# Kernel tuning notes

Hardware: AMD Instinct MI355X
Metric: run time of the kernel (lower is better)

The kernel has to match this reference:

```python
import jax, jax.numpy as jnp
import numpy as np

B, TK, NK, H, E, V = 128, 400, 50, 256, 256, 50000


def setup_inputs() -> dict:
    key = jax.random.key(0)
    ks = iter(jax.random.split(key, 48))
    def rn(shape, s=1.0):
        return jax.random.normal(next(ks), shape, jnp.float32) * s
    def ru(shape):
        return jax.random.uniform(next(ks), shape, jnp.float32)
    z = lambda shape: jnp.zeros(shape, jnp.float32)
    s = 0.05
    inp = {}
    inp['y_t_1'] = jax.random.randint(next(ks), (B,), 0, V)
    inp['h_prev'] = rn((B, H))
    inp['c_prev'] = rn((B, H))
    inp['encoder_outputs'] = rn((B, TK, H))
    inp['encoder_outputs_node'] = rn((B, NK, H))
    inp['enc_padding_mask'] = jnp.ones((B, TK), jnp.float32)
    inp['enc_padding_mask_node'] = jnp.ones((B, NK), jnp.float32)
    inp['c_t_d'] = rn((B, H))
    inp['c_t_g'] = rn((B, H))
    inp['c_t_g2'] = rn((B, H))
    inp['coverage'] = z((B, TK))
    inp['flow'] = ru((B, NK))
    inp['node_to_token'] = ru((B, NK, TK))
    inp['graph'] = ru((B, NK, NK))
    inp['voc_d'] = jax.random.randint(next(ks), (B, TK), 0, V)
    inp['step'] = 0
    # learned parameters
    inp['emb_table'] = rn((V, E), s)
    inp['Wx'] = rn((4 * H, E), s); inp['bx'] = z((E,))
    inp['Wi'] = rn((E, 4 * H), s); inp['Wh'] = rn((H, 4 * H), s)
    inp['bi'] = z((4 * H,)); inp['bh'] = z((4 * H,))
    inp['Whd'] = rn((H, H), s); inp['Wsd'] = rn((2 * H, H), s)
    inp['wcd'] = rn((H,), s); inp['vd'] = rn((H,), s); inp['bd'] = z((H,))
    inp['Wn'] = rn((H, H), s); inp['Wsf'] = rn((2 * H, H), s)
    inp['vf'] = rn((H,), s); inp['bf'] = z((H,))
    inp['Wpg'] = rn((5 * H + E, 1), s); inp['bpg'] = z((1,))
    inp['W1'] = rn((4 * H, H), s); inp['b1'] = z((H,))
    inp['W2'] = rn((H, V), s); inp['b2'] = z((V,))
    return inp


def _forward(y_t_1, h_prev, c_prev, enc, enc_n, mask_t, mask_n, c_t_d, c_t_g, c_t_g2,
             coverage, flow, n2t, graph, voc_d, emb_table, Wx, bx, Wi, Wh, bi, bh,
             Whd, Wsd, wcd, vd, bd, Wn, Wsf, vf, bf, Wpg, bpg, W1, b1, W2, b2):
    sig, tanh = jax.nn.sigmoid, jnp.tanh
    y_emb = emb_table[y_t_1]                                   # [B,E]
    x = jnp.concatenate([c_t_d, c_t_g, c_t_g2, y_emb], 1) @ Wx + bx
    # single-step LSTM (torch gate order i,f,g,o)
    gates = x @ Wi + h_prev @ Wh + bi + bh
    gi, gf, gg, go = jnp.split(gates, 4, axis=1)
    c_new = sig(gf) * c_prev + sig(gi) * tanh(gg)
    h_new = sig(go) * tanh(c_new)
    s_hat = jnp.concatenate([h_new, c_new], 1)                 # [B,2H]
    # doc attention with coverage (Bahdanau)
    e = tanh(enc @ Whd + (s_hat @ Wsd)[:, None, :] + coverage[:, :, None] * wcd + bd) @ vd
    a = jax.nn.softmax(e, axis=1) * mask_t
    a = a / a.sum(1, keepdims=True)                            # [B,TK]
    c_d = jnp.einsum('bt,bth->bh', a, enc)
    coverage_next = coverage + a
    # event-graph node attention (flow-weighted, one-hop propagation)
    en = tanh(enc_n @ Wn + (s_hat @ Wsf)[:, None, :] + bf) @ vf
    an = jax.nn.softmax(en, axis=1) * mask_n
    an = an / an.sum(1, keepdims=True)
    an = an * flow
    an = an / an.sum(1, keepdims=True)                         # [B,NK]
    c_g = jnp.einsum('bn,bnh->bh', an, enc_n)
    an2 = jnp.einsum('bn,bnm->bm', an, graph) * mask_n
    an2 = an2 / an2.sum(1, keepdims=True)
    c_g2 = jnp.einsum('bn,bnh->bh', an2, enc_n)
    a_n2t = jnp.einsum('bn,bnt->bt', an, n2t)
    a_n2t = a_n2t / a_n2t.sum(1, keepdims=True)
    # flow update: per-node max of token attention restricted to node tokens
    flow_ = jnp.max(a[:, None, :] * n2t, axis=2)               # [B,NK]
    flow_next = flow_ / flow_.sum(1, keepdims=True)
    # pointer-generator gate
    p_gen = sig(jnp.concatenate([c_d, c_g, c_g2, s_hat, x], 1) @ Wpg + bpg)  # [B,1]
    out = jnp.concatenate([h_new, c_d, c_g, c_g2], 1) @ W1 + b1
    vocab_dist = jax.nn.softmax(out @ W2 + b2, axis=1)         # [B,V]
    attn_all = a / a.sum(1, keepdims=True)
    attn_ = (1.0 - p_gen) * attn_all
    vocab_ = p_gen * vocab_dist
    rows = jnp.arange(vocab_.shape[0])[:, None]
    final_dist = vocab_.at[rows, voc_d].add(attn_)             # scatter_add over vocab
    return (final_dist, (h_new, c_new), c_d, c_g, c_g2, a, a_n2t, p_gen,
            coverage_next, flow_next)


def reference(y_t_1, h_prev, c_prev, encoder_outputs, encoder_outputs_node,
              enc_padding_mask, enc_padding_mask_node, c_t_d, c_t_g, c_t_g2,
              coverage, flow, node_to_token, graph, voc_d, step,
              emb_table, Wx, bx, Wi, Wh, bi, bh, Whd, Wsd, wcd, vd, bd,
              Wn, Wsf, vf, bf, Wpg, bpg, W1, b1, W2, b2):
    return _forward(y_t_1, h_prev, c_prev, encoder_outputs, encoder_outputs_node,
                    enc_padding_mask, enc_padding_mask_node, c_t_d, c_t_g, c_t_g2,
                    coverage, flow, node_to_token, graph, voc_d, emb_table, Wx, bx,
                    Wi, Wh, bi, bh, Whd, Wsd, wcd, vd, bd, Wn, Wsf, vf, bf,
                    Wpg, bpg, W1, b1, W2, b2)
```

## Files before the change

### kernel.cpp

```cpp
#include <hip/hip_runtime.h>
#include <stdint.h>


typedef unsigned short u16;
typedef unsigned int   u32;

#define Bv  128
#define TKv 400
#define NKv 50
#define Hv  256
#define Vv  50000
#define VPAD 50176
#define NSv 16
#define CHUNKv 3136

typedef __attribute__((ext_vector_type(8))) short bf16x8;
typedef __attribute__((ext_vector_type(4))) float f32x4;

__device__ float g_x[32768];
__device__ float g_xp[4 * 32768];
__device__ float g_gates[131072];
__device__ float g_h[32768];
__device__ float g_c[32768];
__device__ float g_sdp[2 * 32768];
__device__ float g_sfp[2 * 32768];
__device__ float g_e[51200];
__device__ float g_en[6400];
__device__ float g_a[51200];
__device__ float g_cd[32768];
__device__ float g_cdp[2 * 32768];
__device__ float g_cg[32768];
__device__ float g_cg2[32768];
__device__ float g_pg[128];
__device__ float g_o1[32768];
__device__ float g_vred[Bv * NSv * 2];
__device__ float g_logits[6400000];
__device__ u16   g_Wdt[256 * 256];
__device__ u16   g_Wnt[256 * 256];
__device__ u16   g_W2t[(size_t)VPAD * 256];

__device__ __forceinline__ float sigm(float x) { return 1.f / (1.f + expf(-x)); }

__device__ __forceinline__ u16 f2bf(float f) {
    u32 u = __float_as_uint(f);
    return (u16)((u + 0x7fffu + ((u >> 16) & 1u)) >> 16);
}

__device__ __forceinline__ bf16x8 cvt8(const float* __restrict__ p) {
    const float4 a = *(const float4*)p;
    const float4 b = *(const float4*)(p + 4);
    bf16x8 r;
    r[0] = (short)f2bf(a.x); r[1] = (short)f2bf(a.y);
    r[2] = (short)f2bf(a.z); r[3] = (short)f2bf(a.w);
    r[4] = (short)f2bf(b.x); r[5] = (short)f2bf(b.y);
    r[6] = (short)f2bf(b.z); r[7] = (short)f2bf(b.w);
    return r;
}

__device__ __forceinline__ float fast_tanh(float x) {
    x = fminf(fmaxf(x, -15.f), 15.f);
    float e = __expf(2.f * x);
    return (e - 1.f) / (e + 1.f);
}

__device__ __forceinline__ void ms_merge(float& m1, float& s1, float m2, float s2) {
    float M = fmaxf(m1, m2);
    s1 = s1 * expf(m1 - M) + s2 * expf(m2 - M);
    m1 = M;
}

__global__ __launch_bounds__(256) void k_tc(
    const float* __restrict__ src, u16* __restrict__ dst, int K, int N)
{
    __shared__ float tile[32][33];
    const int n0 = blockIdx.x * 32, k0 = blockIdx.y * 32;
    const int tx = threadIdx.x & 31, ty = threadIdx.x >> 5;
    #pragma unroll
    for (int i = 0; i < 32; i += 8) {
        int k = k0 + ty + i, n = n0 + tx;
        tile[ty + i][tx] = (n < N) ? src[(size_t)k * N + n] : 0.f;
    }
    __syncthreads();
    #pragma unroll
    for (int i = 0; i < 32; i += 8) {
        int n = n0 + ty + i, k = k0 + tx;
        dst[(size_t)n * K + k] = f2bf(tile[tx][ty + i]);
    }
}

__global__ __launch_bounds__(256) void k_x(
    const int* __restrict__ y,
    const float* __restrict__ ctd, const float* __restrict__ ctg,
    const float* __restrict__ ctg2, const float* __restrict__ emb,
    const float* __restrict__ Wx)
{
    const int b = blockIdx.x, ks = blockIdx.y, j = threadIdx.x;
    __shared__ float cs[256];
    float v;
    if      (ks == 0) v = ctd [b * 256 + j];
    else if (ks == 1) v = ctg [b * 256 + j];
    else if (ks == 2) v = ctg2[b * 256 + j];
    else              v = emb[(size_t)y[b] * 256 + j];
    cs[j] = v;
    __syncthreads();

    float acc = 0.f;
    const float* w = Wx + (size_t)(ks * 256) * 256 + j;
    #pragma unroll 8
    for (int k = 0; k < 256; k++) acc += cs[k] * w[(size_t)k * 256];
    g_xp[ks * 32768 + b * 256 + j] = acc;
}

__global__ __launch_bounds__(256) void k_gates(
    const float* __restrict__ h_prev,
    const float* __restrict__ Wi, const float* __restrict__ Wh,
    const float* __restrict__ bi, const float* __restrict__ bh,
    const float* __restrict__ bx)
{
    const int b = blockIdx.x, cc = blockIdx.y, j = threadIdx.x;
    __shared__ float xs[256], hs[256];

    float xv = bx[j] + g_xp[b * 256 + j] + g_xp[32768 + b * 256 + j]
             + g_xp[65536 + b * 256 + j] + g_xp[98304 + b * 256 + j];
    xs[j] = xv;
    if (cc == 0) g_x[b * 256 + j] = xv;
    hs[j] = h_prev[b * 256 + j];
    __syncthreads();

    const int col = cc * 256 + j;
    float acc = bi[col] + bh[col];
    const float* wi = Wi + col;
    const float* wh = Wh + col;
    #pragma unroll 8
    for (int k = 0; k < 256; k++)
        acc += xs[k] * wi[(size_t)k * 1024] + hs[k] * wh[(size_t)k * 1024];
    g_gates[b * 1024 + col] = acc;
}

__global__ __launch_bounds__(256) void k_cellsd(
    const float* __restrict__ c_prev,
    const float* __restrict__ Wsd, const float* __restrict__ Wsf,
    float* __restrict__ out_h, float* __restrict__ out_c)
{
    const int b = blockIdx.x, ks = blockIdx.y, j = threadIdx.x;
    __shared__ float sh[256];

    const float* gb = g_gates + b * 1024;
    float gi_ = gb[j], gf_ = gb[256 + j], gg_ = gb[512 + j], go_ = gb[768 + j];
    float cp = c_prev[b * 256 + j];
    float cn = sigm(gf_) * cp + sigm(gi_) * tanhf(gg_);
    float hn = sigm(go_) * tanhf(cn);
    if (ks == 0) {
        g_h[b * 256 + j] = hn;  g_c[b * 256 + j] = cn;
        out_h[b * 256 + j] = hn; out_c[b * 256 + j] = cn;
    }
    sh[j] = (ks == 0) ? hn : cn;
    __syncthreads();

    float asd = 0.f, asf = 0.f;
    const float* wd = Wsd + (size_t)(ks * 256) * 256 + j;
    const float* wf = Wsf + (size_t)(ks * 256) * 256 + j;
    #pragma unroll 8
    for (int k = 0; k < 256; k++) {
        float sv = sh[k];
        asd += sv * wd[(size_t)k * 256];
        asf += sv * wf[(size_t)k * 256];
    }
    g_sdp[ks * 32768 + b * 256 + j] = asd;
    g_sfp[ks * 32768 + b * 256 + j] = asf;
}

__global__ __launch_bounds__(256) void k_scores(
    const float* __restrict__ src, int R,
    const u16* __restrict__ Wt,
    const float* __restrict__ addv0,
    const float* __restrict__ addv1,
    const float* __restrict__ abias,
    const float* __restrict__ cov,
    const float* __restrict__ wcw,
    const float* __restrict__ vv,
    float* __restrict__ eout)
{
    const int b = blockIdx.y, t0 = blockIdx.x * 64;
    const int tid = threadIdx.x;
    const int lane = tid & 63, wave = tid >> 6;
    const int nlow = lane & 15, quad = lane >> 4;

    const u16* brow = Wt + (size_t)(wave * 64 + nlow) * 256 + quad * 8;

    bool tval[4]; const float* arow[4];
    #pragma unroll
    for (int mi = 0; mi < 4; mi++) {
        int trow = t0 + mi * 16 + nlow;
        tval[mi] = trow < R;
        arow[mi] = src + ((size_t)b * R + trow) * 256 + quad * 8;
    }

    const f32x4 zf = {0.f, 0.f, 0.f, 0.f};
    f32x4 acc[4][4];
    #pragma unroll
    for (int mi = 0; mi < 4; mi++)
        #pragma unroll
        for (int ni = 0; ni < 4; ni++) acc[mi][ni] = zf;

    for (int k0 = 0; k0 < 256; k0 += 32) {
        bf16x8 af[4], bf[4];
        #pragma unroll
        for (int mi = 0; mi < 4; mi++) {
            af[mi] = (bf16x8){0, 0, 0, 0, 0, 0, 0, 0};
            if (tval[mi]) af[mi] = cvt8(arow[mi] + k0);
        }
        #pragma unroll
        for (int ni = 0; ni < 4; ni++)
            bf[ni] = *(const bf16x8*)(brow + ni * 4096 + k0);
        #pragma unroll
        for (int mi = 0; mi < 4; mi++)
            #pragma unroll
            for (int ni = 0; ni < 4; ni++)
                acc[mi][ni] = __builtin_amdgcn_mfma_f32_16x16x32_bf16(
                    af[mi], bf[ni], acc[mi][ni], 0, 0, 0);
    }

    __shared__ float part[4][64];
    #pragma unroll
    for (int mi = 0; mi < 4; mi++) {
        float covt[4];
        #pragma unroll
        for (int r = 0; r < 4; r++) {
            int t = t0 + mi * 16 + quad * 4 + r;
            covt[r] = (cov && t < R) ? cov[b * R + t] : 0.f;
        }
        float s4[4] = {0.f, 0.f, 0.f, 0.f};
        #pragma unroll
        for (int ni = 0; ni < 4; ni++) {
            int col = wave * 64 + ni * 16 + nlow;
            float vvc = vv[col];
            float adc = addv0[b * 256 + col] + addv1[b * 256 + col] + abias[col];
            float wcc = wcw ? wcw[col] : 0.f;
            #pragma unroll
            for (int r = 0; r < 4; r++)
                s4[r] += vvc * fast_tanh(acc[mi][ni][r] + adc + covt[r] * wcc);
        }
        #pragma unroll
        for (int r = 0; r < 4; r++) {
            float s = s4[r];
            s += __shfl_xor(s, 1, 64);
            s += __shfl_xor(s, 2, 64);
            s += __shfl_xor(s, 4, 64);
            s += __shfl_xor(s, 8, 64);
            if (nlow == 0) part[wave][mi * 16 + quad * 4 + r] = s;
        }
    }
    __syncthreads();
    if (tid < 64) {
        int t = t0 + tid;
        if (t < R)
            eout[b * R + t] =
                part[0][tid] + part[1][tid] + part[2][tid] + part[3][tid];
    }
}

__global__ __launch_bounds__(256) void k_doc(
    const float* __restrict__ mask,
    const float* __restrict__ cov,
    float* __restrict__ out_a, float* __restrict__ out_cov)
{
    const int b = blockIdx.x, tid = threadIdx.x;
    __shared__ float red[256];

    float e0 = g_e[b * TKv + tid];
    float e1 = (tid + 256 < TKv) ? g_e[b * TKv + tid + 256] : -1e30f;

    float m = fmaxf(e0, e1);
    red[tid] = m; __syncthreads();
    for (int s = 128; s > 0; s >>= 1) { if (tid < s) red[tid] = fmaxf(red[tid], red[tid + s]); __syncthreads(); }
    m = red[0]; __syncthreads();

    float p0 = expf(e0 - m) * mask[b * TKv + tid];
    float p1 = (tid + 256 < TKv) ? expf(e1 - m) * mask[b * TKv + tid + 256] : 0.f;
    red[tid] = p0 + p1; __syncthreads();
    for (int s = 128; s > 0; s >>= 1) { if (tid < s) red[tid] += red[tid + s]; __syncthreads(); }
    float inv = 1.f / red[0];

    float a0 = p0 * inv;
    g_a[b * TKv + tid] = a0;
    out_a[b * TKv + tid] = a0;
    out_cov[b * TKv + tid] = cov[b * TKv + tid] + a0;
    if (tid + 256 < TKv) {
        float a1 = p1 * inv;
        g_a[b * TKv + tid + 256] = a1;
        out_a[b * TKv + tid + 256] = a1;
        out_cov[b * TKv + tid + 256] = cov[b * TKv + tid + 256] + a1;
    }
}

__global__ __launch_bounds__(256) void k_cd(const float* __restrict__ enc)
{
    const int b = blockIdx.x, ks = blockIdx.y, tid = threadIdx.x;
    __shared__ float as_[200];
    if (tid < 200) as_[tid] = g_a[b * TKv + ks * 200 + tid];
    __syncthreads();

    const float* eb = enc + ((size_t)b * TKv + ks * 200) * 256 + tid;
    float acc = 0.f;
    #pragma unroll 8
    for (int t = 0; t < 200; t++) acc += as_[t] * eb[(size_t)t * 256];
    g_cdp[ks * 32768 + b * 256 + tid] = acc;
}

__global__ __launch_bounds__(256) void k_flow(
    const float* __restrict__ n2t, float* __restrict__ out_flow)
{
    const int b = blockIdx.x, tid = threadIdx.x;
    __shared__ float as_[TKv];
    __shared__ float fl[NKv];
    __shared__ float red[256];

    for (int t = tid; t < TKv; t += 256) as_[t] = g_a[b * TKv + t];
    __syncthreads();

    const int nn = tid >> 2, sub = tid & 3;
    float mx = 0.f;
    if (nn < NKv) {
        const float* nb = n2t + ((size_t)b * NKv + nn) * TKv + sub * 100;
        const float* ab = as_ + sub * 100;
        #pragma unroll 4
        for (int t = 0; t < 100; t++) mx = fmaxf(mx, ab[t] * nb[t]);
    }
    mx = fmaxf(mx, __shfl_xor(mx, 1, 64));
    mx = fmaxf(mx, __shfl_xor(mx, 2, 64));
    if (sub == 0 && nn < NKv) fl[nn] = mx;
    __syncthreads();

    float fv = (tid < NKv) ? fl[tid] : 0.f;
    red[tid] = fv; __syncthreads();
    for (int s = 128; s > 0; s >>= 1) { if (tid < s) red[tid] += red[tid + s]; __syncthreads(); }
    float fs = red[0];
    if (tid < NKv) out_flow[b * NKv + tid] = fl[tid] / fs;
}

__global__ __launch_bounds__(256) void k_node1(
    const float* __restrict__ encn,
    const float* __restrict__ maskn,
    const float* __restrict__ flow,
    const float* __restrict__ graph,
    const float* __restrict__ n2t,
    const float* __restrict__ Wpg, const float* __restrict__ bpg,
    float* __restrict__ out_cd, float* __restrict__ out_cg,
    float* __restrict__ out_cg2, float* __restrict__ out_ant,
    float* __restrict__ out_pgen)
{
    const int b = blockIdx.x, tid = threadIdx.x;
    __shared__ float ans[NKv], an2s[NKv], red[256];

    const float cd = g_cdp[b * 256 + tid] + g_cdp[32768 + b * 256 + tid];
    g_cd[b * 256 + tid] = cd;
    out_cd[b * 256 + tid] = cd;

    float v = (tid < NKv) ? g_en[b * NKv + tid] : -1e30f;
    red[tid] = v; __syncthreads();
    for (int s = 128; s > 0; s >>= 1) { if (tid < s) red[tid] = fmaxf(red[tid], red[tid + s]); __syncthreads(); }
    float m = red[0]; __syncthreads();

    float p = (tid < NKv) ? expf(v - m) * maskn[b * NKv + tid] : 0.f;
    red[tid] = p; __syncthreads();
    for (int s = 128; s > 0; s >>= 1) { if (tid < s) red[tid] += red[tid + s]; __syncthreads(); }
    float S = red[0]; __syncthreads();
    p = (tid < NKv) ? (p / S) * flow[b * NKv + tid] : 0.f;
    red[tid] = p; __syncthreads();
    for (int s = 128; s > 0; s >>= 1) { if (tid < s) red[tid] += red[tid + s]; __syncthreads(); }
    float S2 = red[0]; __syncthreads();
    if (tid < NKv) ans[tid] = p / S2;
    __syncthreads();

    float q = 0.f;
    if (tid < NKv) {
        const float* gb = graph + (size_t)b * NKv * NKv + tid;
        #pragma unroll
        for (int n = 0; n < NKv; n++) q += ans[n] * gb[n * NKv];
        q *= maskn[b * NKv + tid];
    }
    red[tid] = q; __syncthreads();
    for (int s = 128; s > 0; s >>= 1) { if (tid < s) red[tid] += red[tid + s]; __syncthreads(); }
    float S3 = red[0]; __syncthreads();
    if (tid < NKv) an2s[tid] = q / S3;
    __syncthreads();

    float cg = 0.f, cg2 = 0.f;
    {
        const float* enb = encn + (size_t)b * NKv * 256 + tid;
        #pragma unroll
        for (int n = 0; n < NKv; n++) {
            float e = enb[n * 256];
            cg  += ans[n]  * e;
            cg2 += an2s[n] * e;
        }
    }
    g_cg[b * 256 + tid] = cg;   out_cg[b * 256 + tid] = cg;
    g_cg2[b * 256 + tid] = cg2; out_cg2[b * 256 + tid] = cg2;

    float at0 = 0.f, at1 = 0.f;
    {
        const float* nb = n2t + (size_t)b * NKv * TKv;
        #pragma unroll
        for (int n = 0; n < NKv; n++) {
            float an = ans[n];
            at0 += an * nb[n * TKv + tid];
            if (tid + 256 < TKv) at1 += an * nb[n * TKv + tid + 256];
        }
    }
    float loc = at0 + ((tid + 256 < TKv) ? at1 : 0.f);
    red[tid] = loc; __syncthreads();
    for (int s = 128; s > 0; s >>= 1) { if (tid < s) red[tid] += red[tid + s]; __syncthreads(); }
    float S4 = red[0]; __syncthreads();
    out_ant[b * TKv + tid] = at0 / S4;
    if (tid + 256 < TKv) out_ant[b * TKv + tid + 256] = at1 / S4;

    float hvv = g_h[b * 256 + tid], cvv = g_c[b * 256 + tid];
    float xvv = g_x[b * 256 + tid];
    float part = cd  * Wpg[tid]        + cg  * Wpg[256 + tid]
               + cg2 * Wpg[512 + tid]  + hvv * Wpg[768 + tid]
               + cvv * Wpg[1024 + tid] + xvv * Wpg[1280 + tid];
    red[tid] = part; __syncthreads();
    for (int s = 128; s > 0; s >>= 1) { if (tid < s) red[tid] += red[tid + s]; __syncthreads(); }
    if (tid == 0) {
        float pg = sigm(red[0] + bpg[0]);
        g_pg[b] = pg; out_pgen[b] = pg;
    }
}

__global__ __launch_bounds__(256) void k_o1(
    const float* __restrict__ W1, const float* __restrict__ b1)
{
    const int b = blockIdx.x, cc = blockIdx.y, tid = threadIdx.x;
    __shared__ float cat[1024];
    __shared__ float red[256];

    cat[tid]       = g_h  [b * 256 + tid];
    cat[256 + tid] = g_cd [b * 256 + tid];
    cat[512 + tid] = g_cg [b * 256 + tid];
    cat[768 + tid] = g_cg2[b * 256 + tid];
    __syncthreads();

    const int lane = tid & 63, kq = tid >> 6;
    const int col = cc * 64 + lane;
    const float* w  = W1 + (size_t)(kq * 256) * 256 + col;
    const float* cs = cat + kq * 256;
    float acc = 0.f;
    #pragma unroll 8
    for (int k = 0; k < 256; k++) acc += cs[k] * w[(size_t)k * 256];
    red[tid] = acc; __syncthreads();

    if (tid < 64) {
        float o = b1[cc * 64 + tid]
                + red[tid] + red[64 + tid] + red[128 + tid] + red[192 + tid];
        g_o1[b * 256 + cc * 64 + tid] = o;
    }
}

__global__ __launch_bounds__(256) void k_logits(const float* __restrict__ b2)
{
    const int v0 = blockIdx.x * 64;
    const int tid = threadIdx.x;
    const int lane = tid & 63, wave = tid >> 6;
    const int nlow = lane & 15, quad = lane >> 4;

    const float* a0p = g_o1 + (wave * 32 + nlow) * 256 + quad * 8;
    const float* a1p = a0p + 16 * 256;
    const u16* bbase = g_W2t + (size_t)(v0 + nlow) * 256 + quad * 8;

    const f32x4 zf = {0.f, 0.f, 0.f, 0.f};
    f32x4 acc0[4], acc1[4];
    #pragma unroll
    for (int i = 0; i < 4; i++) { acc0[i] = zf; acc1[i] = zf; }

    for (int k0 = 0; k0 < 256; k0 += 32) {
        bf16x8 a0 = cvt8(a0p + k0);
        bf16x8 a1 = cvt8(a1p + k0);
        #pragma unroll
        for (int nt = 0; nt < 4; nt++) {
            bf16x8 bf = *(const bf16x8*)(bbase + (size_t)nt * 4096 + k0);
            acc0[nt] = __builtin_amdgcn_mfma_f32_16x16x32_bf16(a0, bf, acc0[nt], 0, 0, 0);
            acc1[nt] = __builtin_amdgcn_mfma_f32_16x16x32_bf16(a1, bf, acc1[nt], 0, 0, 0);
        }
    }

    #pragma unroll
    for (int nt = 0; nt < 4; nt++) {
        int v = v0 + nt * 16 + nlow;
        if (v < Vv) {
            float bb = b2[v];
            #pragma unroll
            for (int r = 0; r < 4; r++) {
                int row0 = wave * 32 + quad * 4 + r;
                g_logits[(size_t)row0 * Vv + v]        = acc0[nt][r] + bb;
                g_logits[(size_t)(row0 + 16) * Vv + v] = acc1[nt][r] + bb;
            }
        }
    }
}

__global__ __launch_bounds__(256) void k_vpart()
{
    const int b = blockIdx.x, ks = blockIdx.y, tid = threadIdx.x;
    __shared__ float rm[256], rs[256];

    const int base = ks * CHUNKv;
    const int end  = min(base + CHUNKv, Vv);
    const int n4   = (end - base) >> 2;
    const float4* L4 = (const float4*)(g_logits + (size_t)b * Vv + base);

    float m = -1e30f, s = 0.f;
    for (int i = tid; i < n4; i += 256) {
        float4 x = L4[i];
        float mx = fmaxf(fmaxf(x.x, x.y), fmaxf(x.z, x.w));
        if (mx > m) { s *= expf(m - mx); m = mx; }
        s += expf(x.x - m) + expf(x.y - m) + expf(x.z - m) + expf(x.w - m);
    }
    rm[tid] = m; rs[tid] = s; __syncthreads();
    for (int off = 128; off > 0; off >>= 1) {
        if (tid < off) {
            float m1 = rm[tid], s1 = rs[tid];
            ms_merge(m1, s1, rm[tid + off], rs[tid + off]);
            rm[tid] = m1; rs[tid] = s1;
        }
        __syncthreads();
    }
    if (tid == 0) {
        g_vred[(b * NSv + ks) * 2]     = rm[0];
        g_vred[(b * NSv + ks) * 2 + 1] = rs[0];
    }
}

__global__ __launch_bounds__(256) void k_vwrite(float* __restrict__ outF)
{
    const int b = blockIdx.x, ks = blockIdx.y, tid = threadIdx.x;

    float M = -1e30f, S = 0.f;
    #pragma unroll
    for (int i = 0; i < NSv; i++) {
        float mi = g_vred[(b * NSv + i) * 2];
        float si = g_vred[(b * NSv + i) * 2 + 1];
        ms_merge(M, S, mi, si);
    }
    const float inv = g_pg[b] / S;

    const int base = ks * CHUNKv;
    const int end  = min(base + CHUNKv, Vv);
    const int n4   = (end - base) >> 2;
    const float4* L4 = (const float4*)(g_logits + (size_t)b * Vv + base);
    float4* O4 = (float4*)(outF + (size_t)b * Vv + base);

    for (int i = tid; i < n4; i += 256) {
        float4 x = L4[i];
        float4 r;
        r.x = expf(x.x - M) * inv;
        r.y = expf(x.y - M) * inv;
        r.z = expf(x.z - M) * inv;
        r.w = expf(x.w - M) * inv;
        O4[i] = r;
    }
}

__global__ __launch_bounds__(256) void k_scatter(
    float* __restrict__ outF, const int* __restrict__ vocd)
{
    const int b = blockIdx.x, tid = threadIdx.x;
    float* Ob = outF + (size_t)b * Vv;
    const float omp = 1.f - g_pg[b];
    for (int t = tid; t < TKv; t += 256)
        atomicAdd(Ob + vocd[b * TKv + t], omp * g_a[b * TKv + t]);
}


extern "C" void kernel_launch(void* const* d_in, const int* in_sizes, int n_in,
                              void* d_out, int out_size, void* d_ws, size_t ws_size,
                              hipStream_t stream)
{
    (void)in_sizes; (void)n_in; (void)out_size; (void)d_ws; (void)ws_size;

    const int*   y      = (const int*)d_in[0];
    const float* h_prev = (const float*)d_in[1];
    const float* c_prev = (const float*)d_in[2];
    const float* enc    = (const float*)d_in[3];
    const float* encn   = (const float*)d_in[4];
    const float* mask   = (const float*)d_in[5];
    const float* maskn  = (const float*)d_in[6];
    const float* ctd    = (const float*)d_in[7];
    const float* ctg    = (const float*)d_in[8];
    const float* ctg2   = (const float*)d_in[9];
    const float* cov    = (const float*)d_in[10];
    const float* flow   = (const float*)d_in[11];
    const float* n2t    = (const float*)d_in[12];
    const float* graph  = (const float*)d_in[13];
    const int*   vocd   = (const int*)d_in[14];
    const float* emb    = (const float*)d_in[16];
    const float* Wx     = (const float*)d_in[17];
    const float* bx     = (const float*)d_in[18];
    const float* Wi     = (const float*)d_in[19];
    const float* Wh     = (const float*)d_in[20];
    const float* bi     = (const float*)d_in[21];
    const float* bh     = (const float*)d_in[22];
    const float* Whd    = (const float*)d_in[23];
    const float* Wsd    = (const float*)d_in[24];
    const float* wcdw   = (const float*)d_in[25];
    const float* vd     = (const float*)d_in[26];
    const float* bd     = (const float*)d_in[27];
    const float* Wn     = (const float*)d_in[28];
    const float* Wsf    = (const float*)d_in[29];
    const float* vf     = (const float*)d_in[30];
    const float* bfv    = (const float*)d_in[31];
    const float* Wpg    = (const float*)d_in[32];
    const float* bpg    = (const float*)d_in[33];
    const float* W1     = (const float*)d_in[34];
    const float* b1     = (const float*)d_in[35];
    const float* W2     = (const float*)d_in[36];
    const float* b2     = (const float*)d_in[37];

    float* o = (float*)d_out;
    float* o_final = o;
    float* o_h     = o + 6400000;
    float* o_c     = o + 6432768;
    float* o_cd    = o + 6465536;
    float* o_cg    = o + 6498304;
    float* o_cg2   = o + 6531072;
    float* o_a     = o + 6563840;
    float* o_ant   = o + 6615040;
    float* o_pg    = o + 6666240;
    float* o_cov   = o + 6666368;
    float* o_fl    = o + 6717568;

    float* g_e_p;   hipGetSymbolAddress((void**)&g_e_p,   HIP_SYMBOL(g_e));
    float* g_en_p;  hipGetSymbolAddress((void**)&g_en_p,  HIP_SYMBOL(g_en));
    float* g_sdp_p; hipGetSymbolAddress((void**)&g_sdp_p, HIP_SYMBOL(g_sdp));
    float* g_sfp_p; hipGetSymbolAddress((void**)&g_sfp_p, HIP_SYMBOL(g_sfp));
    u16*   g_Wdt_p; hipGetSymbolAddress((void**)&g_Wdt_p, HIP_SYMBOL(g_Wdt));
    u16*   g_Wnt_p; hipGetSymbolAddress((void**)&g_Wnt_p, HIP_SYMBOL(g_Wnt));
    u16*   g_W2t_p; hipGetSymbolAddress((void**)&g_W2t_p, HIP_SYMBOL(g_W2t));

    k_tc<<<dim3(8, 8), dim3(256), 0, stream>>>(Whd, g_Wdt_p, 256, 256);
    k_tc<<<dim3(8, 8), dim3(256), 0, stream>>>(Wn,  g_Wnt_p, 256, 256);
    k_tc<<<dim3(VPAD / 32, 8), dim3(256), 0, stream>>>(W2, g_W2t_p, 256, Vv);

    k_x<<<dim3(Bv, 4), dim3(256), 0, stream>>>(y, ctd, ctg, ctg2, emb, Wx);

    k_gates<<<dim3(Bv, 4), dim3(256), 0, stream>>>(h_prev, Wi, Wh, bi, bh, bx);

    k_cellsd<<<dim3(Bv, 2), dim3(256), 0, stream>>>(c_prev, Wsd, Wsf, o_h, o_c);

    k_scores<<<dim3(7, Bv), dim3(256), 0, stream>>>(
        enc, TKv, g_Wdt_p, g_sdp_p, g_sdp_p + 32768, bd, cov, wcdw, vd, g_e_p);

    k_scores<<<dim3(1, Bv), dim3(256), 0, stream>>>(
        encn, NKv, g_Wnt_p, g_sfp_p, g_sfp_p + 32768, bfv,
        nullptr, nullptr, vf, g_en_p);

    k_doc<<<dim3(Bv), dim3(256), 0, stream>>>(mask, cov, o_a, o_cov);

    k_cd<<<dim3(Bv, 2), dim3(256), 0, stream>>>(enc);

    k_flow<<<dim3(Bv), dim3(256), 0, stream>>>(n2t, o_fl);

    k_node1<<<dim3(Bv), dim3(256), 0, stream>>>(
        encn, maskn, flow, graph, n2t, Wpg, bpg,
        o_cd, o_cg, o_cg2, o_ant, o_pg);

    k_o1<<<dim3(Bv, 4), dim3(256), 0, stream>>>(W1, b1);

    k_logits<<<dim3(VPAD / 64), dim3(256), 0, stream>>>(b2);

    k_vpart<<<dim3(Bv, NSv), dim3(256), 0, stream>>>();

    k_vwrite<<<dim3(Bv, NSv), dim3(256), 0, stream>>>(o_final);

    k_scatter<<<dim3(Bv), dim3(256), 0, stream>>>(o_final, vocd);
}
```

Baseline: 529.6 us.

## Pre-convert encoder outputs to bf16, halve score tiles, split context reduction eightfold

Adds a separate kernel that converts encoder outputs (word and node) to bf16 once, so the MFMA score kernel loads packed bf16 directly instead of converting fp32 inline. The score kernel now handles 32 rows per block instead of 64, doubling the grid for more parallelism. The context-vector kernel splits the 400-token reduction into 8 chunks instead of 2, and the partial sums are added up in k_node1. The extra conversion pass reads the full fp32 encoder tensor and writes a bf16 copy, adding memory traffic in exchange for cheaper score loads and higher occupancy.

```diff
diff --git a/kernel.cpp b/kernel.cpp
--- a/kernel.cpp
+++ b/kernel.cpp
@@ -28,7 +28,7 @@
 __device__ float g_en[6400];
 __device__ float g_a[51200];
 __device__ float g_cd[32768];
-__device__ float g_cdp[2 * 32768];
+__device__ float g_cdp[8 * 32768];
 __device__ float g_cg[32768];
 __device__ float g_cg2[32768];
 __device__ float g_pg[128];
@@ -38,6 +38,8 @@
 __device__ u16   g_Wdt[256 * 256];
 __device__ u16   g_Wnt[256 * 256];
 __device__ u16   g_W2t[(size_t)VPAD * 256];
+__device__ u16   g_encb[(size_t)Bv * TKv * 256];
+__device__ u16   g_encnb[(size_t)Bv * NKv * 256];
 
 __device__ __forceinline__ float sigm(float x) { return 1.f / (1.f + expf(-x)); }
 
@@ -69,6 +71,15 @@
     m1 = M;
 }
 
+__global__ __launch_bounds__(256) void k_cvt(
+    const float* __restrict__ src, u16* __restrict__ dst, int n8)
+{
+    int i = blockIdx.x * 256 + threadIdx.x;
+    const int stride = gridDim.x * 256;
+    for (; i < n8; i += stride)
+        *(bf16x8*)(dst + (size_t)i * 8) = cvt8(src + (size_t)i * 8);
+}
+
 __global__ __launch_bounds__(256) void k_tc(
     const float* __restrict__ src, u16* __restrict__ dst, int K, int N)
 {
@@ -171,7 +182,7 @@
 }
 
 __global__ __launch_bounds__(256) void k_scores(
-    const float* __restrict__ src, int R,
+    const u16* __restrict__ srcb, int R,
     const u16* __restrict__ Wt,
     const float* __restrict__ addv0,
     const float* __restrict__ addv1,
@@ -181,49 +192,49 @@
     const float* __restrict__ vv,
     float* __restrict__ eout)
 {
-    const int b = blockIdx.y, t0 = blockIdx.x * 64;
+    const int b = blockIdx.y, t0 = blockIdx.x * 32;
     const int tid = threadIdx.x;
     const int lane = tid & 63, wave = tid >> 6;
     const int nlow = lane & 15, quad = lane >> 4;
 
     const u16* brow = Wt + (size_t)(wave * 64 + nlow) * 256 + quad * 8;
 
-    bool tval[4]; const float* arow[4];
-    #pragma unroll
-    for (int mi = 0; mi < 4; mi++) {
+    bool tval[2]; const u16* arow[2];
+    #pragma unroll
+    for (int mi = 0; mi < 2; mi++) {
         int trow = t0 + mi * 16 + nlow;
         tval[mi] = trow < R;
-        arow[mi] = src + ((size_t)b * R + trow) * 256 + quad * 8;
+        arow[mi] = srcb + ((size_t)b * R + trow) * 256 + quad * 8;
     }
 
     const f32x4 zf = {0.f, 0.f, 0.f, 0.f};
-    f32x4 acc[4][4];
-    #pragma unroll
-    for (int mi = 0; mi < 4; mi++)
+    f32x4 acc[2][4];
+    #pragma unroll
+    for (int mi = 0; mi < 2; mi++)
         #pragma unroll
         for (int ni = 0; ni < 4; ni++) acc[mi][ni] = zf;
 
     for (int k0 = 0; k0 < 256; k0 += 32) {
-        bf16x8 af[4], bf[4];
-        #pragma unroll
-        for (int mi = 0; mi < 4; mi++) {
+        bf16x8 af[2], bf[4];
+        #pragma unroll
+        for (int mi = 0; mi < 2; mi++) {
             af[mi] = (bf16x8){0, 0, 0, 0, 0, 0, 0, 0};
-            if (tval[mi]) af[mi] = cvt8(arow[mi] + k0);
+            if (tval[mi]) af[mi] = *(const bf16x8*)(arow[mi] + k0);
         }
         #pragma unroll
         for (int ni = 0; ni < 4; ni++)
             bf[ni] = *(const bf16x8*)(brow + ni * 4096 + k0);
         #pragma unroll
-        for (int mi = 0; mi < 4; mi++)
+        for (int mi = 0; mi < 2; mi++)
             #pragma unroll
             for (int ni = 0; ni < 4; ni++)
                 acc[mi][ni] = __builtin_amdgcn_mfma_f32_16x16x32_bf16(
                     af[mi], bf[ni], acc[mi][ni], 0, 0, 0);
     }
 
-    __shared__ float part[4][64];
-    #pragma unroll
-    for (int mi = 0; mi < 4; mi++) {
+    __shared__ float part[4][32];
+    #pragma unroll
+    for (int mi = 0; mi < 2; mi++) {
         float covt[4];
         #pragma unroll
         for (int r = 0; r < 4; r++) {
@@ -252,7 +263,7 @@
         }
     }
     __syncthreads();
-    if (tid < 64) {
+    if (tid < 32) {
         int t = t0 + tid;
         if (t < R)
             eout[b * R + t] =
@@ -297,14 +308,14 @@
 __global__ __launch_bounds__(256) void k_cd(const float* __restrict__ enc)
 {
     const int b = blockIdx.x, ks = blockIdx.y, tid = threadIdx.x;
-    __shared__ float as_[200];
-    if (tid < 200) as_[tid] = g_a[b * TKv + ks * 200 + tid];
-    __syncthreads();
-
-    const float* eb = enc + ((size_t)b * TKv + ks * 200) * 256 + tid;
+    __shared__ float as_[50];
+    if (tid < 50) as_[tid] = g_a[b * TKv + ks * 50 + tid];
+    __syncthreads();
+
+    const float* eb = enc + ((size_t)b * TKv + ks * 50) * 256 + tid;
     float acc = 0.f;
-    #pragma unroll 8
-    for (int t = 0; t < 200; t++) acc += as_[t] * eb[(size_t)t * 256];
+    #pragma unroll 10
+    for (int t = 0; t < 50; t++) acc += as_[t] * eb[(size_t)t * 256];
     g_cdp[ks * 32768 + b * 256 + tid] = acc;
 }
 
@@ -353,7 +364,9 @@
     const int b = blockIdx.x, tid = threadIdx.x;
     __shared__ float ans[NKv], an2s[NKv], red[256];
 
-    const float cd = g_cdp[b * 256 + tid] + g_cdp[32768 + b * 256 + tid];
+    float cd = 0.f;
+    #pragma unroll
+    for (int i = 0; i < 8; i++) cd += g_cdp[i * 32768 + b * 256 + tid];
     g_cd[b * 256 + tid] = cd;
     out_cd[b * 256 + tid] = cd;
 
@@ -637,27 +650,32 @@
     u16*   g_Wdt_p; hipGetSymbolAddress((void**)&g_Wdt_p, HIP_SYMBOL(g_Wdt));
     u16*   g_Wnt_p; hipGetSymbolAddress((void**)&g_Wnt_p, HIP_SYMBOL(g_Wnt));
     u16*   g_W2t_p; hipGetSymbolAddress((void**)&g_W2t_p, HIP_SYMBOL(g_W2t));
+    u16*   g_encb_p;  hipGetSymbolAddress((void**)&g_encb_p,  HIP_SYMBOL(g_encb));
+    u16*   g_encnb_p; hipGetSymbolAddress((void**)&g_encnb_p, HIP_SYMBOL(g_encnb));
 
     k_tc<<<dim3(8, 8), dim3(256), 0, stream>>>(Whd, g_Wdt_p, 256, 256);
     k_tc<<<dim3(8, 8), dim3(256), 0, stream>>>(Wn,  g_Wnt_p, 256, 256);
     k_tc<<<dim3(VPAD / 32, 8), dim3(256), 0, stream>>>(W2, g_W2t_p, 256, Vv);
 
+    k_cvt<<<dim3(2048), dim3(256), 0, stream>>>(enc,  g_encb_p,  Bv * TKv * 256 / 8);
+    k_cvt<<<dim3(800),  dim3(256), 0, stream>>>(encn, g_encnb_p, Bv * NKv * 256 / 8);
+
     k_x<<<dim3(Bv, 4), dim3(256), 0, stream>>>(y, ctd, ctg, ctg2, emb, Wx);
 
     k_gates<<<dim3(Bv, 4), dim3(256), 0, stream>>>(h_prev, Wi, Wh, bi, bh, bx);
 
     k_cellsd<<<dim3(Bv, 2), dim3(256), 0, stream>>>(c_prev, Wsd, Wsf, o_h, o_c);
 
-    k_scores<<<dim3(7, Bv), dim3(256), 0, stream>>>(
-        enc, TKv, g_Wdt_p, g_sdp_p, g_sdp_p + 32768, bd, cov, wcdw, vd, g_e_p);
-
-    k_scores<<<dim3(1, Bv), dim3(256), 0, stream>>>(
-        encn, NKv, g_Wnt_p, g_sfp_p, g_sfp_p + 32768, bfv,
+    k_scores<<<dim3(13, Bv), dim3(256), 0, stream>>>(
+        g_encb_p, TKv, g_Wdt_p, g_sdp_p, g_sdp_p + 32768, bd, cov, wcdw, vd, g_e_p);
+
+    k_scores<<<dim3(2, Bv), dim3(256), 0, stream>>>(
+        g_encnb_p, NKv, g_Wnt_p, g_sfp_p, g_sfp_p + 32768, bfv,
         nullptr, nullptr, vf, g_en_p);
 
     k_doc<<<dim3(Bv), dim3(256), 0, stream>>>(mask, cov, o_a, o_cov);
 
-    k_cd<<<dim3(Bv, 2), dim3(256), 0, stream>>>(enc);
+    k_cd<<<dim3(Bv, 8), dim3(256), 0, stream>>>(enc);
 
     k_flow<<<dim3(Bv), dim3(256), 0, stream>>>(n2t, o_fl);
 
```

Measured after the change: 506.3 us. 4.4% less time.
